# Performance work log

Hardware: AMD Instinct MI355X
Metric: run time of the kernel (lower is better)

Reference implementation:

```python
import jax, jax.numpy as jnp
import numpy as np
import math

B, N, F = 16, 1024, 2048


def setup_inputs() -> dict:
    key = jax.random.key(0)
    k_t, k_y = jax.random.split(key)
    # sorted time samples in [0, 100) per batch row
    t = jnp.sort(jax.random.uniform(k_t, (B, N), dtype=jnp.float32) * 100.0, axis=-1)
    y = jax.random.normal(k_y, (B, N), dtype=jnp.float32)
    mask = jnp.ones((B, N), dtype=jnp.float32)
    # monotonically increasing frequency grid (torch.diff in norm requires this)
    freqs = jnp.linspace(1e-5, 5.0, F, dtype=jnp.float32)
    return {"t": t, "y": y, "mask": mask, "freqs": freqs}


def reference(t, y, mask, freqs):
    # t, y, mask: (B, N); freqs: (F,)
    two_pi = 2.0 * math.pi
    omega = two_pi * freqs  # (F,)
    w = omega[None, :, None]          # (1, F, 1)
    tb = t[:, None, :]                # (B, 1, N)
    mb = mask[:, None, :]             # (B, 1, N)
    yb = y[:, None, :]                # (B, 1, N)

    # --- stage 1: tau per (batch, freq) ---
    two_wt = 2.0 * w * tb             # (B, F, N)
    s_sum = jnp.sum(jnp.sin(two_wt) * mb, axis=-1)  # (B, F)
    c_sum = jnp.sum(jnp.cos(two_wt) * mb, axis=-1)  # (B, F)
    tau = jnp.arctan2(s_sum, c_sum) / (2.0 * omega)  # (B, F)

    # --- stage 2: power ---
    wt_tau = w * (tb - tau[:, :, None])  # (B, F, N)
    cos_term = jnp.cos(wt_tau) * mb
    sin_term = jnp.sin(wt_tau) * mb
    p_cos = jnp.sum(yb * cos_term, axis=-1) ** 2 / (jnp.sum(cos_term * cos_term, axis=-1) + 1e-10)
    p_sin = jnp.sum(yb * sin_term, axis=-1) ** 2 / (jnp.sum(sin_term * sin_term, axis=-1) + 1e-10)
    p = 0.5 * (p_cos + p_sin)  # (B, F)

    # --- FAP weighting ---
    m = p.shape[-1]
    fap = 1.0 - (1.0 - jnp.exp(-p)) ** m
    p = p * (1.0 / (fap + 1e-5))

    # --- trapezoidal normalization over the freq grid ---
    df = jnp.diff(freqs)  # (F-1,)
    integral = jnp.sum(0.5 * (p[:, :-1] + p[:, 1:]) * df, axis=-1) + 1e-10  # (B,)
    return p / integral[:, None]
```

## Files before the change

### kernel.cpp

```cpp
#include <hip/hip_runtime.h>
#include <math.h>

#define B_ 16
#define N_ 1024
#define F_ 2048
#define FPB 64
#define SLICES 16
#define NS (N_ / SLICES)
#define NC (NS / 4)

__global__ __launch_bounds__(1024) void ls_power_kernel(
    const float* __restrict__ t,
    const float* __restrict__ y,
    const float* __restrict__ mask,
    const float* __restrict__ freqs,
    float* __restrict__ p_out)
{
    const int tid   = threadIdx.x;
    const int fi    = tid & (FPB - 1);
    const int slice = tid >> 6;
    const int b     = blockIdx.y;
    const int f     = blockIdx.x * FPB + fi;

    const float freq  = freqs[f];
    const float omega = 6.28318530717958647692f * freq;
    const float f2    = 2.0f * freq;

    const int c0 = __builtin_amdgcn_readfirstlane(b * (N_ / 4) + slice * NC);
    const float4* __restrict__ t4 = (const float4*)t;
    const float4* __restrict__ y4 = (const float4*)y;
    const float4* __restrict__ m4 = (const float4*)mask;

    __shared__ float red[SLICES][4][FPB];

    float s_sum = 0.f, c_sum = 0.f;
#pragma unroll 4
    for (int ch = 0; ch < NC; ++ch) {
        float4 tv = t4[c0 + ch];
        float4 mv = m4[c0 + ch];
#pragma unroll
        for (int k = 0; k < 4; ++k) {
            float tn = (&tv.x)[k];
            float mn = (&mv.x)[k];
            float r  = __builtin_amdgcn_fractf(f2 * tn);
            float s  = __builtin_amdgcn_sinf(r);
            float c  = __builtin_amdgcn_cosf(r);
            s_sum = __builtin_fmaf(s, mn, s_sum);
            c_sum = __builtin_fmaf(c, mn, c_sum);
        }
    }
    red[slice][0][fi] = s_sum;
    red[slice][1][fi] = c_sum;
    __syncthreads();

    float S = 0.f, C = 0.f;
#pragma unroll
    for (int k = 0; k < SLICES; ++k) { S += red[k][0][fi]; C += red[k][1][fi]; }
    const float tau = atan2f(S, C) / (2.0f * omega);
    __syncthreads();

    float yc = 0.f, ys = 0.f, cc = 0.f, ss = 0.f;
#pragma unroll 4
    for (int ch = 0; ch < NC; ++ch) {
        float4 tv = t4[c0 + ch];
        float4 yv = y4[c0 + ch];
        float4 mv = m4[c0 + ch];
#pragma unroll
        for (int k = 0; k < 4; ++k) {
            float tn = (&tv.x)[k];
            float yn = (&yv.x)[k];
            float mn = (&mv.x)[k];
            float d  = tn - tau;
            float ph = freq * d;
            float pe = __builtin_fmaf(freq, d, -ph);
            float r  = __builtin_amdgcn_fractf(ph) + pe;
            float s  = __builtin_amdgcn_sinf(r) * mn;
            float c  = __builtin_amdgcn_cosf(r) * mn;
            yc = __builtin_fmaf(yn, c, yc);
            ys = __builtin_fmaf(yn, s, ys);
            cc = __builtin_fmaf(c, c, cc);
            ss = __builtin_fmaf(s, s, ss);
        }
    }
    red[slice][0][fi] = yc;
    red[slice][1][fi] = ys;
    red[slice][2][fi] = cc;
    red[slice][3][fi] = ss;
    __syncthreads();

    if (slice == 0) {
        float YC = 0.f, YS = 0.f, CC = 0.f, SS = 0.f;
#pragma unroll
        for (int k = 0; k < SLICES; ++k) {
            YC += red[k][0][fi];
            YS += red[k][1][fi];
            CC += red[k][2][fi];
            SS += red[k][3][fi];
        }
        float p_cos = (YC * YC) / (CC + 1e-10f);
        float p_sin = (YS * YS) / (SS + 1e-10f);
        float p = 0.5f * (p_cos + p_sin);

        float fap = 1.0f - powf(1.0f - expf(-p), 2048.0f);
        p = p * (1.0f / (fap + 1e-5f));

        p_out[b * F_ + f] = p;
    }
}

__global__ __launch_bounds__(256) void ls_norm_kernel(
    const float* __restrict__ freqs,
    float* __restrict__ p)
{
    const int b   = blockIdx.x;
    const int tid = threadIdx.x;
    float* __restrict__ pb = p + b * F_;

    float local = 0.0f;
    for (int j = tid; j < F_ - 1; j += 256) {
        float df = freqs[j + 1] - freqs[j];
        local += 0.5f * (pb[j] + pb[j + 1]) * df;
    }

    __shared__ float sred[256];
    sred[tid] = local;
    __syncthreads();
    for (int o = 128; o > 0; o >>= 1) {
        if (tid < o) sred[tid] += sred[tid + o];
        __syncthreads();
    }
    const float integral = sred[0] + 1e-10f;

#pragma unroll
    for (int k = 0; k < F_ / 256; ++k) {
        int j = tid + k * 256;
        pb[j] = pb[j] / integral;
    }
}

extern "C" void kernel_launch(void* const* d_in, const int* in_sizes, int n_in,
                              void* d_out, int out_size, void* d_ws, size_t ws_size,
                              hipStream_t stream) {
    const float* t     = (const float*)d_in[0];
    const float* y     = (const float*)d_in[1];
    const float* mask  = (const float*)d_in[2];
    const float* freqs = (const float*)d_in[3];
    float* out = (float*)d_out;

    dim3 grid1(F_ / FPB, B_);
    ls_power_kernel<<<grid1, 1024, 0, stream>>>(t, y, mask, freqs, out);
    ls_norm_kernel<<<B_, 256, 0, stream>>>(freqs, out);
}
```

Baseline: 84.14 us.

## Fuse tau and power passes via angle-addition identities into a single sweep

Replaces the two-pass Lomb-Scargle computation with one pass over the data. Each sample's sin/cos of the base phase is computed once, and double-angle values are derived from it. The kernel accumulates seven moment sums that allow the tau-shifted power terms to be reconstructed afterwards via rotation identities. This removes the second set of transcendental evaluations, the extra global loads and one block barrier. The cost is more reduction traffic in shared memory, plus numerical risk from cancellation in the reconstructed denominators and half-angle square roots.

```diff
diff --git a/kernel.cpp b/kernel.cpp
--- a/kernel.cpp
+++ b/kernel.cpp
@@ -22,83 +22,84 @@
     const int b     = blockIdx.y;
     const int f     = blockIdx.x * FPB + fi;
 
-    const float freq  = freqs[f];
-    const float omega = 6.28318530717958647692f * freq;
-    const float f2    = 2.0f * freq;
+    const float freq = freqs[f];
 
-    const int c0 = __builtin_amdgcn_readfirstlane(b * (N_ / 4) + slice * NC);
+    const int c0i = __builtin_amdgcn_readfirstlane(b * (N_ / 4) + slice * NC);
     const float4* __restrict__ t4 = (const float4*)t;
     const float4* __restrict__ y4 = (const float4*)y;
     const float4* __restrict__ m4 = (const float4*)mask;
 
-    __shared__ float red[SLICES][4][FPB];
+    __shared__ float red[SLICES][7][FPB];
 
-    float s_sum = 0.f, c_sum = 0.f;
+    float S = 0.f, C = 0.f, S2 = 0.f, C2 = 0.f, Sy = 0.f, Cy = 0.f, M2 = 0.f;
+
 #pragma unroll 4
     for (int ch = 0; ch < NC; ++ch) {
-        float4 tv = t4[c0 + ch];
-        float4 mv = m4[c0 + ch];
-#pragma unroll
-        for (int k = 0; k < 4; ++k) {
-            float tn = (&tv.x)[k];
-            float mn = (&mv.x)[k];
-            float r  = __builtin_amdgcn_fractf(f2 * tn);
-            float s  = __builtin_amdgcn_sinf(r);
-            float c  = __builtin_amdgcn_cosf(r);
-            s_sum = __builtin_fmaf(s, mn, s_sum);
-            c_sum = __builtin_fmaf(c, mn, c_sum);
-        }
-    }
-    red[slice][0][fi] = s_sum;
-    red[slice][1][fi] = c_sum;
-    __syncthreads();
-
-    float S = 0.f, C = 0.f;
-#pragma unroll
-    for (int k = 0; k < SLICES; ++k) { S += red[k][0][fi]; C += red[k][1][fi]; }
-    const float tau = atan2f(S, C) / (2.0f * omega);
-    __syncthreads();
-
-    float yc = 0.f, ys = 0.f, cc = 0.f, ss = 0.f;
-#pragma unroll 4
-    for (int ch = 0; ch < NC; ++ch) {
-        float4 tv = t4[c0 + ch];
-        float4 yv = y4[c0 + ch];
-        float4 mv = m4[c0 + ch];
+        float4 tv = t4[c0i + ch];
+        float4 yv = y4[c0i + ch];
+        float4 mv = m4[c0i + ch];
 #pragma unroll
         for (int k = 0; k < 4; ++k) {
             float tn = (&tv.x)[k];
             float yn = (&yv.x)[k];
             float mn = (&mv.x)[k];
-            float d  = tn - tau;
-            float ph = freq * d;
-            float pe = __builtin_fmaf(freq, d, -ph);
+            float ph = freq * tn;
+            float pe = __builtin_fmaf(freq, tn, -ph);
             float r  = __builtin_amdgcn_fractf(ph) + pe;
-            float s  = __builtin_amdgcn_sinf(r) * mn;
-            float c  = __builtin_amdgcn_cosf(r) * mn;
-            yc = __builtin_fmaf(yn, c, yc);
-            ys = __builtin_fmaf(yn, s, ys);
-            cc = __builtin_fmaf(c, c, cc);
-            ss = __builtin_fmaf(s, s, ss);
+            float s0 = __builtin_amdgcn_sinf(r);
+            float cc0 = __builtin_amdgcn_cosf(r);
+            float t1 = s0 * cc0;
+            float s2 = t1 + t1;
+            float u  = s0 + s0;
+            float c2 = __builtin_fmaf(-u, s0, 1.0f);
+            float m2 = mn * mn;
+            float ym = yn * mn;
+            S  = __builtin_fmaf(s2, mn, S);
+            C  = __builtin_fmaf(c2, mn, C);
+            S2 = __builtin_fmaf(s2, m2, S2);
+            C2 = __builtin_fmaf(c2, m2, C2);
+            Sy = __builtin_fmaf(s0, ym, Sy);
+            Cy = __builtin_fmaf(cc0, ym, Cy);
+            M2 += m2;
         }
     }
-    red[slice][0][fi] = yc;
-    red[slice][1][fi] = ys;
-    red[slice][2][fi] = cc;
-    red[slice][3][fi] = ss;
+
+    red[slice][0][fi] = S;
+    red[slice][1][fi] = C;
+    red[slice][2][fi] = S2;
+    red[slice][3][fi] = C2;
+    red[slice][4][fi] = Sy;
+    red[slice][5][fi] = Cy;
+    red[slice][6][fi] = M2;
     __syncthreads();
 
     if (slice == 0) {
-        float YC = 0.f, YS = 0.f, CC = 0.f, SS = 0.f;
+        float rS = 0.f, rC = 0.f, rS2 = 0.f, rC2 = 0.f, rSy = 0.f, rCy = 0.f, rM2 = 0.f;
 #pragma unroll
         for (int k = 0; k < SLICES; ++k) {
-            YC += red[k][0][fi];
-            YS += red[k][1][fi];
-            CC += red[k][2][fi];
-            SS += red[k][3][fi];
+            rS  += red[k][0][fi];
+            rC  += red[k][1][fi];
+            rS2 += red[k][2][fi];
+            rC2 += red[k][3][fi];
+            rSy += red[k][4][fi];
+            rCy += red[k][5][fi];
+            rM2 += red[k][6][fi];
         }
-        float p_cos = (YC * YC) / (CC + 1e-10f);
-        float p_sin = (YS * YS) / (SS + 1e-10f);
+
+        float h      = sqrtf(__builtin_fmaf(rS, rS, rC * rC)) + 1e-30f;
+        float cos2p  = rC / h;
+        float sin2p  = rS / h;
+        float cosp   = sqrtf(0.5f * (1.0f + cos2p));
+        float sinp   = __builtin_copysignf(sqrtf(0.5f * (1.0f - cos2p)), rS);
+
+        float YC = cosp * rCy + sinp * rSy;
+        float YS = cosp * rSy - sinp * rCy;
+        float cross = cos2p * rC2 + sin2p * rS2;
+        float CCd = 0.5f * (rM2 + cross);
+        float SSd = 0.5f * (rM2 - cross);
+
+        float p_cos = (YC * YC) / (CCd + 1e-10f);
+        float p_sin = (YS * YS) / (SSd + 1e-10f);
         float p = 0.5f * (p_cos + p_sin);
 
         float fap = 1.0f - powf(1.0f - expf(-p), 2048.0f);
```

Result: faster. 82.47 us (-2.0%).
